# Kernel optimization log

Measured on AMD Instinct MI355X. Metric: run time of the kernel, lower is better.

Reference implementation:

```python
import jax, jax.numpy as jnp
import numpy as np

N, E = 50000, 600000
DIN, H, DOUT = 128, 128, 64


def setup_inputs() -> dict:
    key = jax.random.key(0)
    ks = jax.random.split(key, 8)
    x = jax.random.normal(ks[0], (N, DIN), dtype=jnp.float32)
    edge_index = jax.random.randint(ks[1], (2, E), 0, N, dtype=jnp.int64)
    s1 = 1.0 / np.sqrt(DIN)
    s2 = 1.0 / np.sqrt(H)
    # PyG SAGEConv: lin_l (on aggregated neighbors, with bias), lin_r (on root, no bias)
    w1_l = jax.random.uniform(ks[2], (DIN, H), jnp.float32, -s1, s1)
    b1 = jnp.zeros((H,), jnp.float32)
    w1_r = jax.random.uniform(ks[3], (DIN, H), jnp.float32, -s1, s1)
    w2_l = jax.random.uniform(ks[4], (H, DOUT), jnp.float32, -s2, s2)
    b2 = jnp.zeros((DOUT,), jnp.float32)
    w2_r = jax.random.uniform(ks[5], (H, DOUT), jnp.float32, -s2, s2)
    return {"x": x, "edge_index": edge_index, "w1_l": w1_l, "b1": b1,
            "w1_r": w1_r, "w2_l": w2_l, "b2": b2, "w2_r": w2_r}


def _sage_conv(h, src, dst, w_l, b, w_r):
    # mean-aggregate neighbor features: gather by src, scatter-sum to dst
    agg = jax.ops.segment_sum(h[src], dst, num_segments=N)  # [N, d]
    deg = jax.ops.segment_sum(jnp.ones((src.shape[0],), h.dtype), dst,
                              num_segments=N)
    mean = agg / jnp.maximum(deg, 1.0)[:, None]
    return mean @ w_l + b + h @ w_r


def reference(x, edge_index, w1_l, b1, w1_r, w2_l, b2, w2_r):
    src, dst = edge_index[0], edge_index[1]
    h = jax.nn.relu(_sage_conv(x, src, dst, w1_l, b1, w1_r))
    return _sage_conv(h, src, dst, w2_l, b2, w2_r)
```

## Files before the change

kernel.cpp:

```cpp
#include <hip/hip_runtime.h>

#define N_NODES 50000
#define N_EDGES 600000
#define DIN 128
#define HD 128
#define DOUT 64
#define NBINS 196
#define BUFCAP 64
#define MAXBIN 6144

typedef float f32x4 __attribute__((ext_vector_type(4)));
typedef short bf16x8 __attribute__((ext_vector_type(8)));

__device__ __forceinline__ unsigned short f2bf(float f) {
    unsigned u = __float_as_uint(f);
    unsigned r = (u + 0x7FFFu + ((u >> 16) & 1u)) >> 16;
    return (unsigned short)r;
}
__device__ __forceinline__ float bf2f(unsigned short s) {
    return __uint_as_float(((unsigned)s) << 16);
}

__global__ __launch_bounds__(256) void prep_kernel(const float* __restrict__ x,
                                                   unsigned short* __restrict__ xb,
                                                   int* __restrict__ binCursor,
                                                   const float* __restrict__ w1l,
                                                   const float* __restrict__ w1r,
                                                   const float* __restrict__ w2l,
                                                   const float* __restrict__ w2r,
                                                   unsigned short* __restrict__ bfr) {
    int gid = blockIdx.x;
    if (gid < 6250) {
        int i = gid * 256 + threadIdx.x;
        float4 v = ((const float4*)x)[i];
        ushort4 o;
        o.x = f2bf(v.x); o.y = f2bf(v.y); o.z = f2bf(v.z); o.w = f2bf(v.w);
        ((ushort4*)xb)[i] = o;
    } else if (gid == 6250) {
        if (threadIdx.x < NBINS) binCursor[threadIdx.x] = threadIdx.x * MAXBIN;
    } else {
        int tid = (gid - 6251) * 256 + threadIdx.x;
        int a = tid >> 14;
        int r = tid & 16383;
        int j = r & 7, lane = (r >> 3) & 63, kc = (r >> 9) & 3, ct = r >> 11;
        int k = kc * 32 + ((lane >> 4) << 3) + j;
        int c = (ct << 4) + (lane & 15);
        float v;
        if (a == 0) v = w1l[k * HD + c];
        else if (a == 1) v = w1r[k * HD + c];
        else v = (c < 64) ? w2l[k * DOUT + c] : w2r[k * DOUT + (c - 64)];
        bfr[tid] = f2bf(v);
    }
}

__global__ __launch_bounds__(256) void binscatter_kernel(const int* __restrict__ ei,
                                                         int* __restrict__ binCursor,
                                                         unsigned* __restrict__ gbuf) {
    __shared__ unsigned buf[NBINS][BUFCAP];
    __shared__ int cnt[NBINS];
    for (int i = threadIdx.x; i < NBINS; i += 256) cnt[i] = 0;
    __syncthreads();
    const int per = (N_EDGES + 255) / 256;
    int beg = blockIdx.x * per;
    int end = min(beg + per, N_EDGES);
    for (int base = beg; base < end; base += 256) {
        int e = base + threadIdx.x;
        if (e < end) {
            int s = ei[e];
            int d = ei[N_EDGES + e];
            int bin = d >> 8;
            unsigned entry = ((unsigned)(d & 255) << 17) | (unsigned)s;
            int pos = atomicAdd(&cnt[bin], 1);
            if (pos < BUFCAP) buf[bin][pos] = entry;
            else { int g = atomicAdd(&binCursor[bin], 1); gbuf[g] = entry; }
        }
        __syncthreads();
        if (threadIdx.x < NBINS) {
            int b = threadIdx.x;
            int n = cnt[b]; if (n > BUFCAP) n = BUFCAP;
            int k = n & ~15;
            if (k > 0) {
                int g = atomicAdd(&binCursor[b], k);
                for (int j = 0; j < k; j++) gbuf[g + j] = buf[b][j];
                for (int j = 0; j < n - k; j++) buf[b][j] = buf[b][k + j];
                cnt[b] = n - k;
            } else {
                cnt[b] = n;
            }
        }
        __syncthreads();
    }
    if (threadIdx.x < NBINS) {
        int b = threadIdx.x;
        int n = cnt[b]; if (n > BUFCAP) n = BUFCAP;
        if (n > 0) {
            int g = atomicAdd(&binCursor[b], n);
            for (int j = 0; j < n; j++) gbuf[g + j] = buf[b][j];
        }
    }
}

__global__ __launch_bounds__(256) void binscan_kernel(const int* __restrict__ binCursor,
                                                      int* __restrict__ binStart,
                                                      int* __restrict__ row_ptr) {
    const int lane = threadIdx.x & 63, wid = threadIdx.x >> 6;
    int i = threadIdx.x;
    int v = (i < NBINS) ? (binCursor[i] - i * MAXBIN) : 0;
    int incl = v;
#pragma unroll
    for (int off = 1; off < 64; off <<= 1) {
        int t = __shfl_up(incl, (unsigned)off, 64);
        if (lane >= off) incl += t;
    }
    __shared__ int ws[4];
    if (lane == 63) ws[wid] = incl;
    __syncthreads();
    int woff = 0;
    for (int w = 0; w < wid; w++) woff += ws[w];
    incl += woff;
    if (i < NBINS) binStart[i] = incl - v;
    if (i == 255) { binStart[NBINS] = incl; row_ptr[N_NODES] = incl; }
}

__global__ __launch_bounds__(256) void binsort_kernel(const unsigned* __restrict__ gbuf,
                                                      const int* __restrict__ binStart,
                                                      int* __restrict__ row_ptr,
                                                      int* __restrict__ csr) {
    __shared__ unsigned ebuf[MAXBIN];
    __shared__ int sorted[MAXBIN];
    __shared__ int hist[256];
    __shared__ int cur[256];
    __shared__ int ws[4];
    const int bin = blockIdx.x;
    const int dst0 = binStart[bin];
    int n = binStart[bin + 1] - dst0;
    if (n > MAXBIN) n = MAXBIN;
    const unsigned* src = gbuf + bin * MAXBIN;
    for (int i = threadIdx.x; i < n; i += 256) ebuf[i] = src[i];
    hist[threadIdx.x] = 0;
    __syncthreads();
    for (int i = threadIdx.x; i < n; i += 256) atomicAdd(&hist[ebuf[i] >> 17], 1);
    __syncthreads();
    const int lane = threadIdx.x & 63, wid = threadIdx.x >> 6;
    int v = hist[threadIdx.x];
    int incl = v;
#pragma unroll
    for (int off = 1; off < 64; off <<= 1) {
        int t = __shfl_up(incl, (unsigned)off, 64);
        if (lane >= off) incl += t;
    }
    if (lane == 63) ws[wid] = incl;
    __syncthreads();
    int woff = 0;
    for (int w = 0; w < wid; w++) woff += ws[w];
    int excl = woff + incl - v;
    cur[threadIdx.x] = excl;
    int node = bin * 256 + threadIdx.x;
    if (node < N_NODES) row_ptr[node] = dst0 + excl;
    __syncthreads();
    for (int i = threadIdx.x; i < n; i += 256) {
        unsigned e = ebuf[i];
        int pos = atomicAdd(&cur[e >> 17], 1);
        sorted[pos] = (int)(e & 0x1FFFFu);
    }
    __syncthreads();
    for (int i = threadIdx.x; i < n; i += 256) csr[dst0 + i] = sorted[i];
}

__global__ __launch_bounds__(256) void gather1_kernel(const int* __restrict__ row_ptr,
                                                      const int* __restrict__ csr,
                                                      const unsigned short* __restrict__ xb,
                                                      unsigned short* __restrict__ meanb) {
    int node = blockIdx.x * 4 + (threadIdx.x >> 6);
    if (node >= N_NODES) return;
    const int lane = threadIdx.x & 63;
    const int g = lane >> 4;
    const int sl = lane & 15;
    int beg = row_ptr[node], end = row_ptr[node + 1];
    float acc[8] = {0.f, 0.f, 0.f, 0.f, 0.f, 0.f, 0.f, 0.f};
    int base = beg + g;
    for (; base + 12 < end; base += 16) {
        int s0 = csr[base];
        int s1 = csr[base + 4];
        int s2 = csr[base + 8];
        int s3 = csr[base + 12];
        uint4 u0 = *(const uint4*)(xb + (size_t)s0 * DIN + sl * 8);
        uint4 u1 = *(const uint4*)(xb + (size_t)s1 * DIN + sl * 8);
        uint4 u2 = *(const uint4*)(xb + (size_t)s2 * DIN + sl * 8);
        uint4 u3 = *(const uint4*)(xb + (size_t)s3 * DIN + sl * 8);
        acc[0] += (__uint_as_float(u0.x << 16) + __uint_as_float(u1.x << 16))
                + (__uint_as_float(u2.x << 16) + __uint_as_float(u3.x << 16));
        acc[1] += (__uint_as_float(u0.x & 0xffff0000u) + __uint_as_float(u1.x & 0xffff0000u))
                + (__uint_as_float(u2.x & 0xffff0000u) + __uint_as_float(u3.x & 0xffff0000u));
        acc[2] += (__uint_as_float(u0.y << 16) + __uint_as_float(u1.y << 16))
                + (__uint_as_float(u2.y << 16) + __uint_as_float(u3.y << 16));
        acc[3] += (__uint_as_float(u0.y & 0xffff0000u) + __uint_as_float(u1.y & 0xffff0000u))
                + (__uint_as_float(u2.y & 0xffff0000u) + __uint_as_float(u3.y & 0xffff0000u));
        acc[4] += (__uint_as_float(u0.z << 16) + __uint_as_float(u1.z << 16))
                + (__uint_as_float(u2.z << 16) + __uint_as_float(u3.z << 16));
        acc[5] += (__uint_as_float(u0.z & 0xffff0000u) + __uint_as_float(u1.z & 0xffff0000u))
                + (__uint_as_float(u2.z & 0xffff0000u) + __uint_as_float(u3.z & 0xffff0000u));
        acc[6] += (__uint_as_float(u0.w << 16) + __uint_as_float(u1.w << 16))
                + (__uint_as_float(u2.w << 16) + __uint_as_float(u3.w << 16));
        acc[7] += (__uint_as_float(u0.w & 0xffff0000u) + __uint_as_float(u1.w & 0xffff0000u))
                + (__uint_as_float(u2.w & 0xffff0000u) + __uint_as_float(u3.w & 0xffff0000u));
    }
    for (; base < end; base += 4) {
        int s0 = csr[base];
        uint4 u = *(const uint4*)(xb + (size_t)s0 * DIN + sl * 8);
        acc[0] += __uint_as_float(u.x << 16);
        acc[1] += __uint_as_float(u.x & 0xffff0000u);
        acc[2] += __uint_as_float(u.y << 16);
        acc[3] += __uint_as_float(u.y & 0xffff0000u);
        acc[4] += __uint_as_float(u.z << 16);
        acc[5] += __uint_as_float(u.z & 0xffff0000u);
        acc[6] += __uint_as_float(u.w << 16);
        acc[7] += __uint_as_float(u.w & 0xffff0000u);
    }
#pragma unroll
    for (int i = 0; i < 8; i++) {
        acc[i] += __shfl_xor(acc[i], 16, 64);
        acc[i] += __shfl_xor(acc[i], 32, 64);
    }
    float r0, r1;
    if (g == 0)      { r0 = acc[0]; r1 = acc[1]; }
    else if (g == 1) { r0 = acc[2]; r1 = acc[3]; }
    else if (g == 2) { r0 = acc[4]; r1 = acc[5]; }
    else             { r0 = acc[6]; r1 = acc[7]; }
    float invd = 1.0f / fmaxf((float)(end - beg), 1.0f);
    ushort2 r; r.x = f2bf(r0 * invd); r.y = f2bf(r1 * invd);
    *(ushort2*)(meanb + (size_t)node * DIN + sl * 8 + g * 2) = r;
}

__global__ __launch_bounds__(256) void fused_kernel(
    const unsigned short* __restrict__ meanb, const unsigned short* __restrict__ xb,
    const unsigned short* __restrict__ B1a, const unsigned short* __restrict__ B1b,
    const unsigned short* __restrict__ B2,
    const float* __restrict__ b1, const float* __restrict__ b2,
    unsigned short* __restrict__ pb, float* __restrict__ out) {
    __shared__ unsigned short Am[64 * 128];
    __shared__ unsigned short Ax[64 * 128];
    const int block0 = blockIdx.x * 64;
    const int tid = threadIdx.x;
    const int lane = tid & 63;
    const int wtile = tid >> 6;

    uint4 mv[4], xv[4];
#pragma unroll
    for (int i = 0; i < 4; i++) {
        int f = tid + i * 256;
        int row = f >> 4;
        int c8 = f & 15;
        int rg = block0 + row;
        if (rg >= N_NODES) rg = N_NODES - 1;
        mv[i] = *(const uint4*)(meanb + (size_t)rg * DIN + c8 * 8);
        xv[i] = *(const uint4*)(xb + (size_t)rg * DIN + c8 * 8);
    }

    f32x4 acc[8];
#pragma unroll
    for (int t = 0; t < 8; t++) acc[t] = (f32x4){0.f, 0.f, 0.f, 0.f};

#pragma unroll
    for (int i = 0; i < 4; i++) {
        int f = tid + i * 256;
        int row = f >> 4;
        int c8 = f & 15;
        int byte = row * 256 + ((c8 * 16) ^ ((row & 7) << 4));
        *(uint4*)((char*)Am + byte) = mv[i];
        *(uint4*)((char*)Ax + byte) = xv[i];
    }

    auto compute = [&](const unsigned short* __restrict__ As,
                       const unsigned short* __restrict__ Bf) {
        const int arow = wtile * 16 + (lane & 15);
        const int swz = (arow & 7) << 4;
#pragma unroll
        for (int kc = 0; kc < 4; kc++) {
            int byte = arow * 256 + ((kc * 64 + ((lane >> 4) << 4)) ^ swz);
            bf16x8 a = *(const bf16x8*)((const char*)As + byte);
#pragma unroll
            for (int ct = 0; ct < 8; ct++) {
                bf16x8 b = *(const bf16x8*)(Bf + ((((ct << 2) + kc) << 6) + lane) * 8);
                acc[ct] = __builtin_amdgcn_mfma_f32_16x16x32_bf16(a, b, acc[ct], 0, 0, 0);
            }
        }
    };

    __syncthreads();
    compute(Am, B1a);
    compute(Ax, B1b);

    {
        const int r0 = wtile * 16 + ((lane >> 4) << 2);
#pragma unroll
        for (int ct = 0; ct < 8; ct++) {
            int col = (ct << 4) + (lane & 15);
            float bv = b1[col];
#pragma unroll
            for (int r = 0; r < 4; r++) {
                float v = fmaxf(acc[ct][r] + bv, 0.f);
                int row = r0 + r;
                int byte = row * 256 + ((col * 2) ^ ((row & 7) << 4));
                *(unsigned short*)((char*)Am + byte) = f2bf(v);
            }
            acc[ct] = (f32x4){0.f, 0.f, 0.f, 0.f};
        }
    }
    compute(Am, B2);

    {
        const int r0 = wtile * 16 + ((lane >> 4) << 2);
#pragma unroll
        for (int ct = 0; ct < 8; ct++) {
            int col = (ct << 4) + (lane & 15);
#pragma unroll
            for (int r = 0; r < 4; r++) {
                int node = block0 + r0 + r;
                if (node < N_NODES) {
                    if (ct < 4) pb[(size_t)node * DOUT + col] = f2bf(acc[ct][r]);
                    else out[(size_t)node * DOUT + (col - 64)] = acc[ct][r] + b2[col - 64];
                }
            }
        }
    }
}

__global__ __launch_bounds__(256) void gather2_kernel(const int* __restrict__ row_ptr,
                                                      const int* __restrict__ csr,
                                                      const unsigned short* __restrict__ pb,
                                                      float* __restrict__ out) {
    int node = blockIdx.x * 4 + (threadIdx.x >> 6);
    if (node >= N_NODES) return;
    const int lane = threadIdx.x & 63;
    const int g = lane >> 3;
    const int sl = lane & 7;
    int beg = row_ptr[node], end = row_ptr[node + 1];
    float acc[8] = {0.f, 0.f, 0.f, 0.f, 0.f, 0.f, 0.f, 0.f};
    int base = beg + g;
    for (; base + 8 < end; base += 16) {
        int s0 = csr[base];
        int s1 = csr[base + 8];
        uint4 u0 = *(const uint4*)(pb + (size_t)s0 * DOUT + sl * 8);
        uint4 u1 = *(const uint4*)(pb + (size_t)s1 * DOUT + sl * 8);
        acc[0] += __uint_as_float(u0.x << 16) + __uint_as_float(u1.x << 16);
        acc[1] += __uint_as_float(u0.x & 0xffff0000u) + __uint_as_float(u1.x & 0xffff0000u);
        acc[2] += __uint_as_float(u0.y << 16) + __uint_as_float(u1.y << 16);
        acc[3] += __uint_as_float(u0.y & 0xffff0000u) + __uint_as_float(u1.y & 0xffff0000u);
        acc[4] += __uint_as_float(u0.z << 16) + __uint_as_float(u1.z << 16);
        acc[5] += __uint_as_float(u0.z & 0xffff0000u) + __uint_as_float(u1.z & 0xffff0000u);
        acc[6] += __uint_as_float(u0.w << 16) + __uint_as_float(u1.w << 16);
        acc[7] += __uint_as_float(u0.w & 0xffff0000u) + __uint_as_float(u1.w & 0xffff0000u);
    }
    if (base < end) {
        int s0 = csr[base];
        uint4 u = *(const uint4*)(pb + (size_t)s0 * DOUT + sl * 8);
        acc[0] += __uint_as_float(u.x << 16);
        acc[1] += __uint_as_float(u.x & 0xffff0000u);
        acc[2] += __uint_as_float(u.y << 16);
        acc[3] += __uint_as_float(u.y & 0xffff0000u);
        acc[4] += __uint_as_float(u.z << 16);
        acc[5] += __uint_as_float(u.z & 0xffff0000u);
        acc[6] += __uint_as_float(u.w << 16);
        acc[7] += __uint_as_float(u.w & 0xffff0000u);
    }
#pragma unroll
    for (int i = 0; i < 8; i++) {
        acc[i] += __shfl_xor(acc[i], 8, 64);
        acc[i] += __shfl_xor(acc[i], 16, 64);
        acc[i] += __shfl_xor(acc[i], 32, 64);
    }
    float r;
    if (g == 0)      r = acc[0];
    else if (g == 1) r = acc[1];
    else if (g == 2) r = acc[2];
    else if (g == 3) r = acc[3];
    else if (g == 4) r = acc[4];
    else if (g == 5) r = acc[5];
    else if (g == 6) r = acc[6];
    else             r = acc[7];
    float invd = 1.0f / fmaxf((float)(end - beg), 1.0f);
    int d = sl * 8 + g;
    out[(size_t)node * DOUT + d] += r * invd;
}

extern "C" void kernel_launch(void* const* d_in, const int* in_sizes, int n_in,
                              void* d_out, int out_size, void* d_ws, size_t ws_size,
                              hipStream_t stream) {
    const float* x   = (const float*)d_in[0];
    const int*   ei  = (const int*)d_in[1];
    const float* w1l = (const float*)d_in[2];
    const float* b1  = (const float*)d_in[3];
    const float* w1r = (const float*)d_in[4];
    const float* w2l = (const float*)d_in[5];
    const float* b2  = (const float*)d_in[6];
    const float* w2r = (const float*)d_in[7];
    float* out = (float*)d_out;

    int* iw = (int*)d_ws;
    int* binCursor = iw;
    int* binStart  = iw + 196;
    int* row_ptr   = iw + 400;
    int* csr       = iw + 50401;
    unsigned* gbuf = (unsigned*)(iw + 650404);
    unsigned short* meanb = (unsigned short*)(iw + 1854632);
    unsigned short* xb  = meanb + (size_t)N_NODES * DIN;
    unsigned short* pbb = xb + (size_t)N_NODES * DIN;
    unsigned short* bfr = pbb + (size_t)N_NODES * DOUT;
    const unsigned short* B1a = bfr;
    const unsigned short* B1b = bfr + 16384;
    const unsigned short* B2  = bfr + 32768;

    prep_kernel<<<6443, 256, 0, stream>>>(x, xb, binCursor, w1l, w1r, w2l, w2r, bfr);
    binscatter_kernel<<<256, 256, 0, stream>>>(ei, binCursor, gbuf);
    binscan_kernel<<<1, 256, 0, stream>>>(binCursor, binStart, row_ptr);
    binsort_kernel<<<NBINS, 256, 0, stream>>>(gbuf, binStart, row_ptr, csr);

    gather1_kernel<<<(N_NODES + 3) / 4, 256, 0, stream>>>(row_ptr, csr, xb, meanb);
    fused_kernel<<<(N_NODES + 63) / 64, 256, 0, stream>>>(meanb, xb, B1a, B1b, B2,
                                                          b1, b2, pbb, out);
    gather2_kernel<<<(N_NODES + 3) / 4, 256, 0, stream>>>(row_ptr, csr, pbb, out);
}
```

Baseline: 128.1 us.

## Fuse edge binning into the prep kernel and sort the CSR in place

Edge bin-scatter now runs in the same launch as the bf16 conversion of x and the weights, inside one mega kernel. A tiny cursor-init kernel replaces the separate init block. The global scan kernel is removed: binsort writes each bin's sorted indices in place inside its fixed-capacity gbuf slot and emits per-node begin and end pointers, so the compacted csr array and the shared-memory sorted buffer go away. The gather loops are restructured to use masked loads with no separate tail loop, and the shared staging buffer is halved, which should help occupancy when scatter blocks share the GPU with conversion blocks. In exchange, gathers read from a sparse padded layout, and the smaller buffer means more edges take the slow path of one global atomic per edge.

```diff
diff --git a/kernel.cpp b/kernel.cpp
--- a/kernel.cpp
+++ b/kernel.cpp
@@ -6,7 +6,7 @@
 #define HD 128
 #define DOUT 64
 #define NBINS 196
-#define BUFCAP 64
+#define BUFCAP 32
 #define MAXBIN 6144
 
 typedef float f32x4 __attribute__((ext_vector_type(4)));
@@ -17,29 +17,73 @@
     unsigned r = (u + 0x7FFFu + ((u >> 16) & 1u)) >> 16;
     return (unsigned short)r;
 }
-__device__ __forceinline__ float bf2f(unsigned short s) {
-    return __uint_as_float(((unsigned)s) << 16);
-}
-
-__global__ __launch_bounds__(256) void prep_kernel(const float* __restrict__ x,
+
+__global__ __launch_bounds__(256) void cursorinit_kernel(int* __restrict__ binCursor) {
+    if (threadIdx.x < NBINS) binCursor[threadIdx.x] = threadIdx.x * MAXBIN;
+}
+
+__global__ __launch_bounds__(256) void mega_kernel(const int* __restrict__ ei,
+                                                   int* __restrict__ binCursor,
+                                                   unsigned* __restrict__ gbuf,
+                                                   const float* __restrict__ x,
                                                    unsigned short* __restrict__ xb,
-                                                   int* __restrict__ binCursor,
                                                    const float* __restrict__ w1l,
                                                    const float* __restrict__ w1r,
                                                    const float* __restrict__ w2l,
                                                    const float* __restrict__ w2r,
                                                    unsigned short* __restrict__ bfr) {
     int gid = blockIdx.x;
-    if (gid < 6250) {
-        int i = gid * 256 + threadIdx.x;
+    if (gid < 256) {
+        __shared__ unsigned buf[NBINS][BUFCAP];
+        __shared__ int cnt[NBINS];
+        for (int i = threadIdx.x; i < NBINS; i += 256) cnt[i] = 0;
+        __syncthreads();
+        const int per = (N_EDGES + 255) / 256;
+        int beg = gid * per;
+        int end = min(beg + per, N_EDGES);
+        for (int base = beg; base < end; base += 256) {
+            int e = base + threadIdx.x;
+            if (e < end) {
+                int s = ei[e];
+                int d = ei[N_EDGES + e];
+                int bin = d >> 8;
+                unsigned entry = ((unsigned)(d & 255) << 17) | (unsigned)s;
+                int pos = atomicAdd(&cnt[bin], 1);
+                if (pos < BUFCAP) buf[bin][pos] = entry;
+                else { int g = atomicAdd(&binCursor[bin], 1); gbuf[g] = entry; }
+            }
+            __syncthreads();
+            if (threadIdx.x < NBINS) {
+                int b = threadIdx.x;
+                int n = cnt[b]; if (n > BUFCAP) n = BUFCAP;
+                int k = n & ~15;
+                if (k > 0) {
+                    int g = atomicAdd(&binCursor[b], k);
+                    for (int j = 0; j < k; j++) gbuf[g + j] = buf[b][j];
+                    for (int j = 0; j < n - k; j++) buf[b][j] = buf[b][k + j];
+                    cnt[b] = n - k;
+                } else {
+                    cnt[b] = n;
+                }
+            }
+            __syncthreads();
+        }
+        if (threadIdx.x < NBINS) {
+            int b = threadIdx.x;
+            int n = cnt[b]; if (n > BUFCAP) n = BUFCAP;
+            if (n > 0) {
+                int g = atomicAdd(&binCursor[b], n);
+                for (int j = 0; j < n; j++) gbuf[g + j] = buf[b][j];
+            }
+        }
+    } else if (gid < 6506) {
+        int i = (gid - 256) * 256 + threadIdx.x;
         float4 v = ((const float4*)x)[i];
         ushort4 o;
         o.x = f2bf(v.x); o.y = f2bf(v.y); o.z = f2bf(v.z); o.w = f2bf(v.w);
         ((ushort4*)xb)[i] = o;
-    } else if (gid == 6250) {
-        if (threadIdx.x < NBINS) binCursor[threadIdx.x] = threadIdx.x * MAXBIN;
     } else {
-        int tid = (gid - 6251) * 256 + threadIdx.x;
+        int tid = (gid - 6506) * 256 + threadIdx.x;
         int a = tid >> 14;
         int r = tid & 16383;
         int j = r & 7, lane = (r >> 3) & 63, kc = (r >> 9) & 3, ct = r >> 11;
@@ -53,89 +97,19 @@
     }
 }
 
-__global__ __launch_bounds__(256) void binscatter_kernel(const int* __restrict__ ei,
-                                                         int* __restrict__ binCursor,
-                                                         unsigned* __restrict__ gbuf) {
-    __shared__ unsigned buf[NBINS][BUFCAP];
-    __shared__ int cnt[NBINS];
-    for (int i = threadIdx.x; i < NBINS; i += 256) cnt[i] = 0;
-    __syncthreads();
-    const int per = (N_EDGES + 255) / 256;
-    int beg = blockIdx.x * per;
-    int end = min(beg + per, N_EDGES);
-    for (int base = beg; base < end; base += 256) {
-        int e = base + threadIdx.x;
-        if (e < end) {
-            int s = ei[e];
-            int d = ei[N_EDGES + e];
-            int bin = d >> 8;
-            unsigned entry = ((unsigned)(d & 255) << 17) | (unsigned)s;
-            int pos = atomicAdd(&cnt[bin], 1);
-            if (pos < BUFCAP) buf[bin][pos] = entry;
-            else { int g = atomicAdd(&binCursor[bin], 1); gbuf[g] = entry; }
-        }
-        __syncthreads();
-        if (threadIdx.x < NBINS) {
-            int b = threadIdx.x;
-            int n = cnt[b]; if (n > BUFCAP) n = BUFCAP;
-            int k = n & ~15;
-            if (k > 0) {
-                int g = atomicAdd(&binCursor[b], k);
-                for (int j = 0; j < k; j++) gbuf[g + j] = buf[b][j];
-                for (int j = 0; j < n - k; j++) buf[b][j] = buf[b][k + j];
-                cnt[b] = n - k;
-            } else {
-                cnt[b] = n;
-            }
-        }
-        __syncthreads();
-    }
-    if (threadIdx.x < NBINS) {
-        int b = threadIdx.x;
-        int n = cnt[b]; if (n > BUFCAP) n = BUFCAP;
-        if (n > 0) {
-            int g = atomicAdd(&binCursor[b], n);
-            for (int j = 0; j < n; j++) gbuf[g + j] = buf[b][j];
-        }
-    }
-}
-
-__global__ __launch_bounds__(256) void binscan_kernel(const int* __restrict__ binCursor,
-                                                      int* __restrict__ binStart,
-                                                      int* __restrict__ row_ptr) {
-    const int lane = threadIdx.x & 63, wid = threadIdx.x >> 6;
-    int i = threadIdx.x;
-    int v = (i < NBINS) ? (binCursor[i] - i * MAXBIN) : 0;
-    int incl = v;
-#pragma unroll
-    for (int off = 1; off < 64; off <<= 1) {
-        int t = __shfl_up(incl, (unsigned)off, 64);
-        if (lane >= off) incl += t;
-    }
-    __shared__ int ws[4];
-    if (lane == 63) ws[wid] = incl;
-    __syncthreads();
-    int woff = 0;
-    for (int w = 0; w < wid; w++) woff += ws[w];
-    incl += woff;
-    if (i < NBINS) binStart[i] = incl - v;
-    if (i == 255) { binStart[NBINS] = incl; row_ptr[N_NODES] = incl; }
-}
-
-__global__ __launch_bounds__(256) void binsort_kernel(const unsigned* __restrict__ gbuf,
-                                                      const int* __restrict__ binStart,
+__global__ __launch_bounds__(256) void binsort_kernel(unsigned* __restrict__ gbuf,
+                                                      const int* __restrict__ binCursor,
                                                       int* __restrict__ row_ptr,
-                                                      int* __restrict__ csr) {
+                                                      int* __restrict__ row_end) {
     __shared__ unsigned ebuf[MAXBIN];
-    __shared__ int sorted[MAXBIN];
     __shared__ int hist[256];
     __shared__ int cur[256];
     __shared__ int ws[4];
     const int bin = blockIdx.x;
-    const int dst0 = binStart[bin];
-    int n = binStart[bin + 1] - dst0;
+    const int base = bin * MAXBIN;
+    int n = binCursor[bin] - base;
     if (n > MAXBIN) n = MAXBIN;
-    const unsigned* src = gbuf + bin * MAXBIN;
+    unsigned* src = gbuf + base;
     for (int i = threadIdx.x; i < n; i += 256) ebuf[i] = src[i];
     hist[threadIdx.x] = 0;
     __syncthreads();
@@ -156,18 +130,20 @@
     int excl = woff + incl - v;
     cur[threadIdx.x] = excl;
     int node = bin * 256 + threadIdx.x;
-    if (node < N_NODES) row_ptr[node] = dst0 + excl;
+    if (node < N_NODES) {
+        row_ptr[node] = base + excl;
+        row_end[node] = base + excl + v;
+    }
     __syncthreads();
     for (int i = threadIdx.x; i < n; i += 256) {
         unsigned e = ebuf[i];
         int pos = atomicAdd(&cur[e >> 17], 1);
-        sorted[pos] = (int)(e & 0x1FFFFu);
-    }
-    __syncthreads();
-    for (int i = threadIdx.x; i < n; i += 256) csr[dst0 + i] = sorted[i];
+        src[pos] = e & 0x1FFFFu;
+    }
 }
 
 __global__ __launch_bounds__(256) void gather1_kernel(const int* __restrict__ row_ptr,
+                                                      const int* __restrict__ row_end,
                                                       const int* __restrict__ csr,
                                                       const unsigned short* __restrict__ xb,
                                                       unsigned short* __restrict__ meanb) {
@@ -176,46 +152,26 @@
     const int lane = threadIdx.x & 63;
     const int g = lane >> 4;
     const int sl = lane & 15;
-    int beg = row_ptr[node], end = row_ptr[node + 1];
+    int beg = row_ptr[node], end = row_end[node];
     float acc[8] = {0.f, 0.f, 0.f, 0.f, 0.f, 0.f, 0.f, 0.f};
-    int base = beg + g;
-    for (; base + 12 < end; base += 16) {
+    for (int base = beg + g; base < end; base += 12) {
+        int i1 = base + 4, i2 = base + 8;
         int s0 = csr[base];
-        int s1 = csr[base + 4];
-        int s2 = csr[base + 8];
-        int s3 = csr[base + 12];
+        int s1 = csr[i1 < end ? i1 : base];
+        int s2 = csr[i2 < end ? i2 : base];
         uint4 u0 = *(const uint4*)(xb + (size_t)s0 * DIN + sl * 8);
         uint4 u1 = *(const uint4*)(xb + (size_t)s1 * DIN + sl * 8);
         uint4 u2 = *(const uint4*)(xb + (size_t)s2 * DIN + sl * 8);
-        uint4 u3 = *(const uint4*)(xb + (size_t)s3 * DIN + sl * 8);
-        acc[0] += (__uint_as_float(u0.x << 16) + __uint_as_float(u1.x << 16))
-                + (__uint_as_float(u2.x << 16) + __uint_as_float(u3.x << 16));
-        acc[1] += (__uint_as_float(u0.x & 0xffff0000u) + __uint_as_float(u1.x & 0xffff0000u))
-                + (__uint_as_float(u2.x & 0xffff0000u) + __uint_as_float(u3.x & 0xffff0000u));
-        acc[2] += (__uint_as_float(u0.y << 16) + __uint_as_float(u1.y << 16))
-                + (__uint_as_float(u2.y << 16) + __uint_as_float(u3.y << 16));
-        acc[3] += (__uint_as_float(u0.y & 0xffff0000u) + __uint_as_float(u1.y & 0xffff0000u))
-                + (__uint_as_float(u2.y & 0xffff0000u) + __uint_as_float(u3.y & 0xffff0000u));
-        acc[4] += (__uint_as_float(u0.z << 16) + __uint_as_float(u1.z << 16))
-                + (__uint_as_float(u2.z << 16) + __uint_as_float(u3.z << 16));
-        acc[5] += (__uint_as_float(u0.z & 0xffff0000u) + __uint_as_float(u1.z & 0xffff0000u))
-                + (__uint_as_float(u2.z & 0xffff0000u) + __uint_as_float(u3.z & 0xffff0000u));
-        acc[6] += (__uint_as_float(u0.w << 16) + __uint_as_float(u1.w << 16))
-                + (__uint_as_float(u2.w << 16) + __uint_as_float(u3.w << 16));
-        acc[7] += (__uint_as_float(u0.w & 0xffff0000u) + __uint_as_float(u1.w & 0xffff0000u))
-                + (__uint_as_float(u2.w & 0xffff0000u) + __uint_as_float(u3.w & 0xffff0000u));
-    }
-    for (; base < end; base += 4) {
-        int s0 = csr[base];
-        uint4 u = *(const uint4*)(xb + (size_t)s0 * DIN + sl * 8);
-        acc[0] += __uint_as_float(u.x << 16);
-        acc[1] += __uint_as_float(u.x & 0xffff0000u);
-        acc[2] += __uint_as_float(u.y << 16);
-        acc[3] += __uint_as_float(u.y & 0xffff0000u);
-        acc[4] += __uint_as_float(u.z << 16);
-        acc[5] += __uint_as_float(u.z & 0xffff0000u);
-        acc[6] += __uint_as_float(u.w << 16);
-        acc[7] += __uint_as_float(u.w & 0xffff0000u);
+        if (i1 >= end) u1 = (uint4){0u, 0u, 0u, 0u};
+        if (i2 >= end) u2 = (uint4){0u, 0u, 0u, 0u};
+        acc[0] += __uint_as_float(u0.x << 16) + __uint_as_float(u1.x << 16) + __uint_as_float(u2.x << 16);
+        acc[1] += __uint_as_float(u0.x & 0xffff0000u) + __uint_as_float(u1.x & 0xffff0000u) + __uint_as_float(u2.x & 0xffff0000u);
+        acc[2] += __uint_as_float(u0.y << 16) + __uint_as_float(u1.y << 16) + __uint_as_float(u2.y << 16);
+        acc[3] += __uint_as_float(u0.y & 0xffff0000u) + __uint_as_float(u1.y & 0xffff0000u) + __uint_as_float(u2.y & 0xffff0000u);
+        acc[4] += __uint_as_float(u0.z << 16) + __uint_as_float(u1.z << 16) + __uint_as_float(u2.z << 16);
+        acc[5] += __uint_as_float(u0.z & 0xffff0000u) + __uint_as_float(u1.z & 0xffff0000u) + __uint_as_float(u2.z & 0xffff0000u);
+        acc[6] += __uint_as_float(u0.w << 16) + __uint_as_float(u1.w << 16) + __uint_as_float(u2.w << 16);
+        acc[7] += __uint_as_float(u0.w & 0xffff0000u) + __uint_as_float(u1.w & 0xffff0000u) + __uint_as_float(u2.w & 0xffff0000u);
     }
 #pragma unroll
     for (int i = 0; i < 8; i++) {
@@ -327,6 +283,7 @@
 }
 
 __global__ __launch_bounds__(256) void gather2_kernel(const int* __restrict__ row_ptr,
+                                                      const int* __restrict__ row_end,
                                                       const int* __restrict__ csr,
                                                       const unsigned short* __restrict__ pb,
                                                       float* __restrict__ out) {
@@ -335,14 +292,15 @@
     const int lane = threadIdx.x & 63;
     const int g = lane >> 3;
     const int sl = lane & 7;
-    int beg = row_ptr[node], end = row_ptr[node + 1];
+    int beg = row_ptr[node], end = row_end[node];
     float acc[8] = {0.f, 0.f, 0.f, 0.f, 0.f, 0.f, 0.f, 0.f};
-    int base = beg + g;
-    for (; base + 8 < end; base += 16) {
+    for (int base = beg + g; base < end; base += 16) {
+        int i1 = base + 8;
         int s0 = csr[base];
-        int s1 = csr[base + 8];
+        int s1 = csr[i1 < end ? i1 : base];
         uint4 u0 = *(const uint4*)(pb + (size_t)s0 * DOUT + sl * 8);
         uint4 u1 = *(const uint4*)(pb + (size_t)s1 * DOUT + sl * 8);
+        if (i1 >= end) u1 = (uint4){0u, 0u, 0u, 0u};
         acc[0] += __uint_as_float(u0.x << 16) + __uint_as_float(u1.x << 16);
         acc[1] += __uint_as_float(u0.x & 0xffff0000u) + __uint_as_float(u1.x & 0xffff0000u);
         acc[2] += __uint_as_float(u0.y << 16) + __uint_as_float(u1.y << 16);
@@ -351,18 +309,6 @@
         acc[5] += __uint_as_float(u0.z & 0xffff0000u) + __uint_as_float(u1.z & 0xffff0000u);
         acc[6] += __uint_as_float(u0.w << 16) + __uint_as_float(u1.w << 16);
         acc[7] += __uint_as_float(u0.w & 0xffff0000u) + __uint_as_float(u1.w & 0xffff0000u);
-    }
-    if (base < end) {
-        int s0 = csr[base];
-        uint4 u = *(const uint4*)(pb + (size_t)s0 * DOUT + sl * 8);
-        acc[0] += __uint_as_float(u.x << 16);
-        acc[1] += __uint_as_float(u.x & 0xffff0000u);
-        acc[2] += __uint_as_float(u.y << 16);
-        acc[3] += __uint_as_float(u.y & 0xffff0000u);
-        acc[4] += __uint_as_float(u.z << 16);
-        acc[5] += __uint_as_float(u.z & 0xffff0000u);
-        acc[6] += __uint_as_float(u.w << 16);
-        acc[7] += __uint_as_float(u.w & 0xffff0000u);
     }
 #pragma unroll
     for (int i = 0; i < 8; i++) {
@@ -399,11 +345,10 @@
 
     int* iw = (int*)d_ws;
     int* binCursor = iw;
-    int* binStart  = iw + 196;
-    int* row_ptr   = iw + 400;
-    int* csr       = iw + 50401;
-    unsigned* gbuf = (unsigned*)(iw + 650404);
-    unsigned short* meanb = (unsigned short*)(iw + 1854632);
+    int* row_ptr   = iw + 256;
+    int* row_end   = iw + 50256;
+    unsigned* gbuf = (unsigned*)(iw + 100352);
+    unsigned short* meanb = (unsigned short*)(iw + 1304576);
     unsigned short* xb  = meanb + (size_t)N_NODES * DIN;
     unsigned short* pbb = xb + (size_t)N_NODES * DIN;
     unsigned short* bfr = pbb + (size_t)N_NODES * DOUT;
@@ -411,13 +356,15 @@
     const unsigned short* B1b = bfr + 16384;
     const unsigned short* B2  = bfr + 32768;
 
-    prep_kernel<<<6443, 256, 0, stream>>>(x, xb, binCursor, w1l, w1r, w2l, w2r, bfr);
-    binscatter_kernel<<<256, 256, 0, stream>>>(ei, binCursor, gbuf);
-    binscan_kernel<<<1, 256, 0, stream>>>(binCursor, binStart, row_ptr);
-    binsort_kernel<<<NBINS, 256, 0, stream>>>(gbuf, binStart, row_ptr, csr);
-
-    gather1_kernel<<<(N_NODES + 3) / 4, 256, 0, stream>>>(row_ptr, csr, xb, meanb);
+    cursorinit_kernel<<<1, 256, 0, stream>>>(binCursor);
+    mega_kernel<<<6698, 256, 0, stream>>>(ei, binCursor, gbuf, x, xb,
+                                          w1l, w1r, w2l, w2r, bfr);
+    binsort_kernel<<<NBINS, 256, 0, stream>>>(gbuf, binCursor, row_ptr, row_end);
+
+    gather1_kernel<<<(N_NODES + 3) / 4, 256, 0, stream>>>(row_ptr, row_end,
+                                                          (const int*)gbuf, xb, meanb);
     fused_kernel<<<(N_NODES + 63) / 64, 256, 0, stream>>>(meanb, xb, B1a, B1b, B2,
                                                           b1, b2, pbb, out);
-    gather2_kernel<<<(N_NODES + 3) / 4, 256, 0, stream>>>(row_ptr, csr, pbb, out);
-}
+    gather2_kernel<<<(N_NODES + 3) / 4, 256, 0, stream>>>(row_ptr, row_end,
+                                                          (const int*)gbuf, pbb, out);
+}
```

Result: faster. 115.4 us (median of 2 runs) (-9.9%).
